# Kernel optimization log

Hardware: AMD Instinct MI355X
Metric: run time of the kernel (lower is better)

## Reference

```python
import jax, jax.numpy as jnp
import numpy as np

N = 100000      # nodes
E = 1600000     # edges
HID = 128
NODE_IN = 32
EDGE_IN = 16
EMB = 32
VOCAB = 100000
LAYERS = 3
EPS = 1e-5


def setup_inputs() -> dict:
    key = jax.random.key(0)
    ks = jax.random.split(key, 24)
    s = 0.05
    inp = {
        "x": jax.random.normal(ks[0], (N, NODE_IN), jnp.float32),
        "edge_attr": jax.random.normal(ks[1], (E, EDGE_IN), jnp.float32),
        "naics_emb": jax.random.normal(ks[2], (VOCAB, EMB), jnp.float32) * s,
        "ln_g": jnp.ones((EMB,), jnp.float32),
        "ln_b": jnp.zeros((EMB,), jnp.float32),
        "W_in": jax.random.normal(ks[3], (EMB + NODE_IN, HID), jnp.float32) * s,
        "b_in": jnp.zeros((HID,), jnp.float32),
        "Wl": jax.random.normal(ks[4], (LAYERS, HID, HID), jnp.float32) * s,
        "bl": jnp.zeros((LAYERS, HID), jnp.float32),
        "Wr": jax.random.normal(ks[5], (LAYERS, HID, HID), jnp.float32) * s,
        "bn_g": jnp.ones((LAYERS, HID), jnp.float32),
        "bn_b": jnp.zeros((LAYERS, HID), jnp.float32),
        "We1": jax.random.normal(ks[6], (2 * HID + EDGE_IN, HID), jnp.float32) * s,
        "be1": jnp.zeros((HID,), jnp.float32),
        "We2": jax.random.normal(ks[7], (HID, HID // 2), jnp.float32) * s,
        "be2": jnp.zeros((HID // 2,), jnp.float32),
        "We3": jax.random.normal(ks[8], (HID // 2, 1), jnp.float32) * s,
        "be3": jnp.zeros((1,), jnp.float32),
        "edge_index": jax.random.randint(ks[9], (2, E), 0, N, jnp.int64 if jax.config.jax_enable_x64 else jnp.int32),
        "naics_indices": jax.random.randint(ks[10], (N,), 0, VOCAB, jnp.int64 if jax.config.jax_enable_x64 else jnp.int32),
    }
    return inp


def reference(x, edge_attr, naics_emb, ln_g, ln_b, W_in, b_in, Wl, bl, Wr,
              bn_g, bn_b, We1, be1, We2, be2, We3, be3, edge_index, naics_indices):
    # NAICS embedding + LayerNorm
    emb = naics_emb[naics_indices]                    # [N, EMB]
    mu = emb.mean(-1, keepdims=True)
    var = emb.var(-1, keepdims=True)
    emb = (emb - mu) * jax.lax.rsqrt(var + EPS) * ln_g + ln_b

    # input projection (dropout in eval mode = identity)
    h = jax.nn.relu(jnp.concatenate([emb, x], axis=1) @ W_in + b_in)  # [N, HID]
    initial = h

    row, col = edge_index[0], edge_index[1]           # src, dst (PyG: aggregate at dst)
    deg = jax.ops.segment_sum(jnp.ones((E,), h.dtype), col, num_segments=N)
    inv_deg = (1.0 / jnp.maximum(deg, 1.0))[:, None]  # [N,1]

    for i in range(LAYERS):
        # SAGEConv: lin_l(mean_j x_j) + lin_r(x_i)
        agg = jax.ops.segment_sum(h[row], col, num_segments=N) * inv_deg
        out = agg @ Wl[i] + bl[i] + h @ Wr[i]
        # BatchNorm1d (training-mode batch statistics over nodes)
        m = out.mean(0)
        v = out.var(0)
        out = (out - m) * jax.lax.rsqrt(v + EPS) * bn_g[i] + bn_b[i]
        h = jnp.tanh(out) + h                         # activation + residual
        if i % 2 == 1:
            h = h + initial

    # edge-gather MLP
    ef = jnp.concatenate([h[row], h[col], edge_attr], axis=1)  # [E, 2H+EDGE_IN]
    z = jax.nn.relu(ef @ We1 + be1)
    z = jax.nn.relu(z @ We2 + be2)
    return z @ We3 + be3                              # [E, 1]
```

## Files before the change

### kernel.cpp

```cpp
#include <hip/hip_runtime.h>
#include <hip/hip_bf16.h>
#include <cstddef>

#define HID 128
#define EMBD 32
#define NIN 32
#define EIN 16
#define EPSV 1e-5f

__device__ __forceinline__ float rlf(float v, int l) {
    return __int_as_float(__builtin_amdgcn_readlane(__float_as_int(v), l));
}

extern "C" __global__ void __launch_bounds__(256)
k_input(const float* __restrict__ x, const float* __restrict__ etab,
        const int* __restrict__ nidx, const float* __restrict__ lng_,
        const float* __restrict__ lnb_, const float* __restrict__ Win,
        const float* __restrict__ bin_, float* __restrict__ h,
        float* __restrict__ init_, int nn)
{
    __shared__ float Ws[64 * HID];
    __shared__ float lng[EMBD], lnb[EMBD], bin[HID];
    __shared__ float xbuf[4][64];
    for (int i = threadIdx.x; i < 64 * HID; i += 256) Ws[i] = Win[i];
    if (threadIdx.x < EMBD) { lng[threadIdx.x] = lng_[threadIdx.x]; lnb[threadIdx.x] = lnb_[threadIdx.x]; }
    if (threadIdx.x < HID) bin[threadIdx.x] = bin_[threadIdx.x];
    __syncthreads();
    const int wv = threadIdx.x >> 6, lane = threadIdx.x & 63;
    const int w0 = blockIdx.x * 4 + wv, nw = gridDim.x * 4;
    for (int n = w0; n < nn; n += nw) {
        float e = 0.f;
        if (lane < EMBD) e = etab[(size_t)nidx[n] * EMBD + lane];
        float s = e, q = e * e;
        #pragma unroll
        for (int o = 16; o; o >>= 1) { s += __shfl_xor(s, o, 32); q += __shfl_xor(q, o, 32); }
        if (lane < EMBD) {
            float m = s * (1.f / EMBD);
            float v = q * (1.f / EMBD) - m * m;
            xbuf[wv][lane] = (e - m) * rsqrtf(v + EPSV) * lng[lane] + lnb[lane];
        } else {
            xbuf[wv][lane] = x[(size_t)n * NIN + (lane - NIN)];
        }
        float2 a0 = *(const float2*)&bin[2 * lane], a1 = {0.f, 0.f};
        #pragma unroll 8
        for (int k = 0; k < 64; k += 2) {
            float2 wA = *(const float2*)&Ws[k * HID + 2 * lane];
            float2 wB = *(const float2*)&Ws[(k + 1) * HID + 2 * lane];
            a0.x = fmaf(xbuf[wv][k], wA.x, a0.x);     a0.y = fmaf(xbuf[wv][k], wA.y, a0.y);
            a1.x = fmaf(xbuf[wv][k + 1], wB.x, a1.x); a1.y = fmaf(xbuf[wv][k + 1], wB.y, a1.y);
        }
        float2 r; r.x = fmaxf(a0.x + a1.x, 0.f); r.y = fmaxf(a0.y + a1.y, 0.f);
        *(float2*)&h[(size_t)n * HID + 2 * lane] = r;
        *(float2*)&init_[(size_t)n * HID + 2 * lane] = r;
    }
}

extern "C" __global__ void k_deg(const int* __restrict__ col, int* __restrict__ degi, int ne) {
    int i = blockIdx.x * blockDim.x + threadIdx.x, st = gridDim.x * blockDim.x;
    for (; i < ne; i += st) atomicAdd(&degi[col[i]], 1);
}

extern "C" __global__ void __launch_bounds__(1024)
k_scan(const int* __restrict__ degi, int* __restrict__ offs, int nn) {
    __shared__ int ps[1024];
    const int t = threadIdx.x;
    const int per = (nn + 1023) / 1024;
    const int s = min(t * per, nn), e = min(s + per, nn);
    int sum = 0;
    for (int i = s; i < e; i++) sum += degi[i];
    ps[t] = sum;
    __syncthreads();
    for (int off = 1; off < 1024; off <<= 1) {
        int v = (t >= off) ? ps[t - off] : 0;
        __syncthreads();
        ps[t] += v;
        __syncthreads();
    }
    int run = (t ? ps[t - 1] : 0);
    for (int i = s; i < e; i++) { offs[i] = run; run += degi[i]; }
    if (t == 1023) offs[nn] = run;
}

extern "C" __global__ void k_fill(const int* __restrict__ row, const int* __restrict__ col,
                                  const int* __restrict__ offs, int* __restrict__ cur,
                                  int* __restrict__ csr, int ne) {
    int i = blockIdx.x * blockDim.x + threadIdx.x, st = gridDim.x * blockDim.x;
    for (; i < ne; i += st) {
        int c = col[i];
        int p = atomicAdd(&cur[c], 1);
        csr[offs[c] + p] = row[i];
    }
}

extern "C" __global__ void __launch_bounds__(256)
k_agg(const float* __restrict__ h, const int* __restrict__ offs,
      const int* __restrict__ csr, float* __restrict__ agg, int nn)
{
    const int lane = threadIdx.x & 63;
    int w = blockIdx.x * 4 + (threadIdx.x >> 6), nw = gridDim.x * 4;
    for (int n = w; n < nn; n += nw) {
        const int nu = __builtin_amdgcn_readfirstlane(n);
        const int o0 = offs[nu], o1 = offs[nu + 1];
        float2 acc = {0.f, 0.f};
        int j = o0;
        for (; j + 4 <= o1; j += 4) {
            int s0 = csr[j], s1 = csr[j + 1], s2 = csr[j + 2], s3 = csr[j + 3];
            float2 v0 = *(const float2*)&h[(size_t)s0 * HID + 2 * lane];
            float2 v1 = *(const float2*)&h[(size_t)s1 * HID + 2 * lane];
            float2 v2 = *(const float2*)&h[(size_t)s2 * HID + 2 * lane];
            float2 v3 = *(const float2*)&h[(size_t)s3 * HID + 2 * lane];
            acc.x += (v0.x + v1.x) + (v2.x + v3.x);
            acc.y += (v0.y + v1.y) + (v2.y + v3.y);
        }
        for (; j < o1; j++) {
            int s0 = csr[j];
            float2 v0 = *(const float2*)&h[(size_t)s0 * HID + 2 * lane];
            acc.x += v0.x; acc.y += v0.y;
        }
        const float idg = 1.f / fmaxf((float)(o1 - o0), 1.f);
        float2 r; r.x = acc.x * idg; r.y = acc.y * idg;
        *(float2*)&agg[(size_t)n * HID + 2 * lane] = r;
    }
}

extern "C" __global__ void k_degf(const int* __restrict__ col, float* __restrict__ deg, int ne) {
    int i = blockIdx.x * blockDim.x + threadIdx.x, st = gridDim.x * blockDim.x;
    for (; i < ne; i += st) unsafeAtomicAdd(&deg[col[i]], 1.f);
}
extern "C" __global__ void k_invdeg(const float* __restrict__ deg, float* __restrict__ inv, int nn) {
    int i = blockIdx.x * blockDim.x + threadIdx.x;
    if (i < nn) inv[i] = 1.f / fmaxf(deg[i], 1.f);
}
extern "C" __global__ void __launch_bounds__(256)
k_scatter(const float* __restrict__ h, const int* __restrict__ row,
          const int* __restrict__ col, float* agg, int ne)
{
    const int lane = threadIdx.x & 63;
    int w = blockIdx.x * 4 + (threadIdx.x >> 6), nw = gridDim.x * 4;
    for (int e = w; e < ne; e += nw) {
        int r = row[e], c = col[e];
        float2 v = *(const float2*)&h[(size_t)r * HID + 2 * lane];
        unsafeAtomicAdd(&agg[(size_t)c * HID + 2 * lane], v.x);
        unsafeAtomicAdd(&agg[(size_t)c * HID + 2 * lane + 1], v.y);
    }
}

extern "C" __global__ void __launch_bounds__(512)
k_gemm(const float* __restrict__ X1, const float* __restrict__ scale,
       const float* __restrict__ W1, const float* __restrict__ X2,
       const float* __restrict__ W2, const float* __restrict__ bias,
       float* __restrict__ out, float* __restrict__ stats, int nn)
{
    __shared__ float W1s[HID * HID];
    __shared__ float W2s[HID * HID];
    const int tid = threadIdx.x;
    const bool dual = (X2 != nullptr);
    for (int i = tid; i < HID * HID / 4; i += 512) {
        ((float4*)W1s)[i] = ((const float4*)W1)[i];
        if (dual) ((float4*)W2s)[i] = ((const float4*)W2)[i];
    }
    __syncthreads();
    const int lane = tid & 63, wv = tid >> 6;
    const int gw = blockIdx.x * 8 + wv, nwv = gridDim.x * 8;
    float2 bv = {0.f, 0.f};
    if (bias) bv = *(const float2*)&bias[2 * lane];
    float2 sm = {0.f, 0.f}, sq = {0.f, 0.f};
    for (int nb = gw * 8; nb < nn; nb += nwv * 8) {
        const int nN = min(8, nn - nb);
        float2 xA[8], xB[8];
        #pragma unroll
        for (int i = 0; i < 8; i++) {
            xA[i] = {0.f, 0.f}; xB[i] = {0.f, 0.f};
            if (i < nN) {
                xA[i] = *(const float2*)&X1[(size_t)(nb + i) * HID + 2 * lane];
                if (scale) { float sc = scale[nb + i]; xA[i].x *= sc; xA[i].y *= sc; }
                if (dual) xB[i] = *(const float2*)&X2[(size_t)(nb + i) * HID + 2 * lane];
            }
        }
        float2 acc[8];
        #pragma unroll
        for (int i = 0; i < 8; i++) acc[i] = bv;
        if (dual) {
            for (int k = 0; k < HID; k += 2) {
                float2 w1a = *(const float2*)&W1s[k * HID + 2 * lane];
                float2 w1b = *(const float2*)&W1s[(k + 1) * HID + 2 * lane];
                float2 w2a = *(const float2*)&W2s[k * HID + 2 * lane];
                float2 w2b = *(const float2*)&W2s[(k + 1) * HID + 2 * lane];
                const int kl = k >> 1;
                #pragma unroll
                for (int i = 0; i < 8; i++) {
                    float sa = rlf(xA[i].x, kl), sb = rlf(xA[i].y, kl);
                    float ta = rlf(xB[i].x, kl), tb = rlf(xB[i].y, kl);
                    acc[i].x = fmaf(sa, w1a.x, acc[i].x); acc[i].y = fmaf(sa, w1a.y, acc[i].y);
                    acc[i].x = fmaf(sb, w1b.x, acc[i].x); acc[i].y = fmaf(sb, w1b.y, acc[i].y);
                    acc[i].x = fmaf(ta, w2a.x, acc[i].x); acc[i].y = fmaf(ta, w2a.y, acc[i].y);
                    acc[i].x = fmaf(tb, w2b.x, acc[i].x); acc[i].y = fmaf(tb, w2b.y, acc[i].y);
                }
            }
        } else {
            for (int k = 0; k < HID; k += 2) {
                float2 w1a = *(const float2*)&W1s[k * HID + 2 * lane];
                float2 w1b = *(const float2*)&W1s[(k + 1) * HID + 2 * lane];
                const int kl = k >> 1;
                #pragma unroll
                for (int i = 0; i < 8; i++) {
                    float sa = rlf(xA[i].x, kl), sb = rlf(xA[i].y, kl);
                    acc[i].x = fmaf(sa, w1a.x, acc[i].x); acc[i].y = fmaf(sa, w1a.y, acc[i].y);
                    acc[i].x = fmaf(sb, w1b.x, acc[i].x); acc[i].y = fmaf(sb, w1b.y, acc[i].y);
                }
            }
        }
        #pragma unroll
        for (int i = 0; i < 8; i++) {
            if (i < nN) {
                *(float2*)&out[(size_t)(nb + i) * HID + 2 * lane] = acc[i];
                if (stats) {
                    sm.x += acc[i].x; sm.y += acc[i].y;
                    sq.x += acc[i].x * acc[i].x; sq.y += acc[i].y * acc[i].y;
                }
            }
        }
    }
    if (stats) {
        unsafeAtomicAdd(&stats[2 * lane],           sm.x);
        unsafeAtomicAdd(&stats[2 * lane + 1],       sm.y);
        unsafeAtomicAdd(&stats[HID + 2 * lane],     sq.x);
        unsafeAtomicAdd(&stats[HID + 2 * lane + 1], sq.y);
    }
}

extern "C" __global__ void k_bnfin(const float* __restrict__ stats, const float* __restrict__ g,
                                   const float* __restrict__ b, float* __restrict__ scsh, float invn)
{
    int f = threadIdx.x;
    if (f < HID) {
        float m = stats[f] * invn;
        float v = stats[HID + f] * invn - m * m;
        float s = rsqrtf(v + EPSV) * g[f];
        scsh[f] = s;
        scsh[HID + f] = fmaf(-m, s, b[f]);
    }
}

extern "C" __global__ void __launch_bounds__(256)
k_update(const float* __restrict__ outb, const float* __restrict__ scsh,
         float* h, const float* __restrict__ init_, int addinit, int n4)
{
    int i = blockIdx.x * blockDim.x + threadIdx.x, st = gridDim.x * blockDim.x;
    for (; i < n4; i += st) {
        float4 o = ((const float4*)outb)[i];
        int f = (i & 31) * 4;
        float4 s  = *(const float4*)&scsh[f];
        float4 sh = *(const float4*)&scsh[HID + f];
        float4 hv = ((const float4*)h)[i];
        float4 r;
        r.x = tanhf(fmaf(o.x, s.x, sh.x)) + hv.x;
        r.y = tanhf(fmaf(o.y, s.y, sh.y)) + hv.y;
        r.z = tanhf(fmaf(o.z, s.z, sh.z)) + hv.z;
        r.w = tanhf(fmaf(o.w, s.w, sh.w)) + hv.w;
        if (addinit) {
            float4 iv = ((const float4*)init_)[i];
            r.x += iv.x; r.y += iv.y; r.z += iv.z; r.w += iv.w;
        }
        ((float4*)h)[i] = r;
    }
}

extern "C" __global__ void __launch_bounds__(256)
k_edge(const float* __restrict__ A, const float* __restrict__ B,
       const float* __restrict__ eattr, const int* __restrict__ row,
       const int* __restrict__ col, const float* __restrict__ We1e,
       const float* __restrict__ We2, const float* __restrict__ be2,
       const float* __restrict__ We3, const float* __restrict__ be3,
       float* __restrict__ outp, int ne)
{
    __shared__ float zbuf[32][132];
    __shared__ float tbuf[4][32][8];
    const int tid = threadIdx.x, lane = tid & 63, wv = tid >> 6;
    float2 w1r[16];
    #pragma unroll
    for (int j = 0; j < 16; j++) w1r[j] = *(const float2*)&We1e[j * HID + 2 * lane];
    const int fi = lane & 7, ks = lane >> 3;
    const int f0 = 16 * wv + 2 * fi;
    float w2r0[16], w2r1[16];
    #pragma unroll
    for (int m = 0; m < 16; m++) {
        w2r0[m] = We2[(16 * ks + m) * 64 + f0];
        w2r1[m] = We2[(16 * ks + m) * 64 + f0 + 1];
    }
    const float b20 = be2[f0], b21 = be2[f0 + 1];
    const float w30 = We3[f0], w31 = We3[f0 + 1];
    const float bias3 = be3[0];
    const int wcol4 = (((lane >> 1) & 3) << 3) | ((lane >> 1) >> 2);
    const int woff = wcol4 * 4 + (lane & 1) * 2;
    for (int cb = blockIdx.x * 32; cb < ne; cb += gridDim.x * 32) {
        const int e0 = cb + wv * 8;
        float2 ear = {0.f, 0.f};
        if (e0 + (lane >> 3) < ne) ear = *(const float2*)&eattr[(size_t)e0 * EIN + 2 * lane];
        int rr[8], cc[8];
        #pragma unroll
        for (int i = 0; i < 8; i++) {
            const int e = e0 + i;
            rr[i] = (e < ne) ? row[e] : 0;
            cc[i] = (e < ne) ? col[e] : 0;
        }
        float2 av[8], bv8[8];
        #pragma unroll
        for (int i = 0; i < 8; i++) {
            av[i]  = *(const float2*)&A[(size_t)rr[i] * HID + 2 * lane];
            bv8[i] = *(const float2*)&B[(size_t)cc[i] * HID + 2 * lane];
        }
        #pragma unroll
        for (int i = 0; i < 8; i++) {
            float2 q; q.x = av[i].x + bv8[i].x; q.y = av[i].y + bv8[i].y;
            #pragma unroll
            for (int j = 0; j < 16; j++) {
                float s = rlf((j & 1) ? ear.y : ear.x, i * 8 + (j >> 1));
                q.x = fmaf(s, w1r[j].x, q.x);
                q.y = fmaf(s, w1r[j].y, q.y);
            }
            q.x = fmaxf(q.x, 0.f); q.y = fmaxf(q.y, 0.f);
            *(float2*)&zbuf[wv * 8 + i][woff] = q;
        }
        __syncthreads();
        #pragma unroll 2
        for (int e = 0; e < 32; e++) {
            float acc0 = 0.f, acc1 = 0.f;
            #pragma unroll
            for (int t = 0; t < 4; t++) {
                float4 z = *(const float4*)&zbuf[e][(t * 8 + ks) * 4];
                acc0 = fmaf(z.x, w2r0[4 * t + 0], acc0);
                acc0 = fmaf(z.y, w2r0[4 * t + 1], acc0);
                acc0 = fmaf(z.z, w2r0[4 * t + 2], acc0);
                acc0 = fmaf(z.w, w2r0[4 * t + 3], acc0);
                acc1 = fmaf(z.x, w2r1[4 * t + 0], acc1);
                acc1 = fmaf(z.y, w2r1[4 * t + 1], acc1);
                acc1 = fmaf(z.z, w2r1[4 * t + 2], acc1);
                acc1 = fmaf(z.w, w2r1[4 * t + 3], acc1);
            }
            acc0 += __shfl_xor(acc0, 8);  acc1 += __shfl_xor(acc1, 8);
            acc0 += __shfl_xor(acc0, 16); acc1 += __shfl_xor(acc1, 16);
            acc0 += __shfl_xor(acc0, 32); acc1 += __shfl_xor(acc1, 32);
            float o0 = fmaxf(acc0 + b20, 0.f), o1 = fmaxf(acc1 + b21, 0.f);
            float t3 = fmaf(o0, w30, o1 * w31);
            if (ks == 0) tbuf[wv][e][fi] = t3;
        }
        __syncthreads();
        {
            const int e = tid >> 3, p = tid & 7;
            float s = (tbuf[0][e][p] + tbuf[1][e][p]) + (tbuf[2][e][p] + tbuf[3][e][p]);
            s += __shfl_xor(s, 1); s += __shfl_xor(s, 2); s += __shfl_xor(s, 4);
            if (p == 0 && cb + e < ne) outp[cb + e] = s + bias3;
        }
        __syncthreads();
    }
}

extern "C" void kernel_launch(void* const* d_in, const int* in_sizes, int n_in,
                              void* d_out, int out_size, void* d_ws, size_t ws_size,
                              hipStream_t stream)
{
    const float* x     = (const float*)d_in[0];
    const float* eattr = (const float*)d_in[1];
    const float* etab  = (const float*)d_in[2];
    const float* lng   = (const float*)d_in[3];
    const float* lnb   = (const float*)d_in[4];
    const float* Win   = (const float*)d_in[5];
    const float* bin   = (const float*)d_in[6];
    const float* Wl    = (const float*)d_in[7];
    const float* bl    = (const float*)d_in[8];
    const float* Wr    = (const float*)d_in[9];
    const float* bng   = (const float*)d_in[10];
    const float* bnb   = (const float*)d_in[11];
    const float* We1   = (const float*)d_in[12];
    const float* be1   = (const float*)d_in[13];
    const float* We2   = (const float*)d_in[14];
    const float* be2   = (const float*)d_in[15];
    const float* We3   = (const float*)d_in[16];
    const float* be3   = (const float*)d_in[17];
    const int*   eidx  = (const int*)d_in[18];
    const int*   nidx  = (const int*)d_in[19];

    const int nn = in_sizes[0] / NIN;
    const int ne = in_sizes[1] / EIN;
    const int* row = eidx;
    const int* col = eidx + ne;

    float* ws = (float*)d_ws;
    const size_t big = (size_t)nn * HID;
    float* h    = ws;
    float* bufB = ws + big;
    float* bufA = ws + 2 * big;
    float* tail = ws + 3 * big;

    const size_t need_csr = (3 * big + 3 * (size_t)nn + 1 + (size_t)ne + 512) * 4;
    const bool use_csr = (ws_size >= need_csr);

    k_input<<<512, 256, 0, stream>>>(x, etab, nidx, lng, lnb, Win, bin, h, bufB, nn);

    if (use_csr) {
        int*   degi  = (int*)tail;
        int*   offs  = degi + nn;
        int*   cur   = offs + nn + 1;
        int*   csr   = cur + nn;
        float* stats = (float*)(csr + ne);
        float* scsh  = stats + 2 * HID;

        hipMemsetAsync(degi, 0, (size_t)nn * 4, stream);
        hipMemsetAsync(cur, 0, (size_t)nn * 4, stream);
        k_deg<<<1024, 256, 0, stream>>>(col, degi, ne);
        k_scan<<<1, 1024, 0, stream>>>(degi, offs, nn);
        k_fill<<<1024, 256, 0, stream>>>(row, col, offs, cur, csr, ne);

        for (int i = 0; i < 3; i++) {
            hipMemsetAsync(stats, 0, 2 * HID * 4, stream);
            k_agg<<<2048, 256, 0, stream>>>(h, offs, csr, bufA, nn);
            k_gemm<<<256, 512, 0, stream>>>(bufA, nullptr, Wl + (size_t)i * HID * HID,
                                            h, Wr + (size_t)i * HID * HID, bl + i * HID,
                                            bufA, stats, nn);
            k_bnfin<<<1, 128, 0, stream>>>(stats, bng + i * HID, bnb + i * HID, scsh, 1.0f / nn);
            k_update<<<1024, 256, 0, stream>>>(bufA, scsh, h, bufB, i & 1, nn * HID / 4);
        }

        k_gemm<<<256, 512, 0, stream>>>(h, nullptr, We1, nullptr, nullptr, be1, bufA, nullptr, nn);
        k_gemm<<<256, 512, 0, stream>>>(h, nullptr, We1 + HID * HID, nullptr, nullptr, nullptr, bufB, nullptr, nn);
    } else {
        float* deg   = tail;
        float* inv   = deg + nn;
        float* stats = inv + nn;
        float* scsh  = stats + 2 * HID;

        hipMemsetAsync(deg, 0, (size_t)nn * 4, stream);
        k_degf<<<1024, 256, 0, stream>>>(col, deg, ne);
        k_invdeg<<<(nn + 255) / 256, 256, 0, stream>>>(deg, inv, nn);

        for (int i = 0; i < 3; i++) {
            hipMemsetAsync(bufA, 0, big * 4, stream);
            hipMemsetAsync(stats, 0, 2 * HID * 4, stream);
            k_scatter<<<2048, 256, 0, stream>>>(h, row, col, bufA, ne);
            k_gemm<<<256, 512, 0, stream>>>(bufA, inv, Wl + (size_t)i * HID * HID,
                                            h, Wr + (size_t)i * HID * HID, bl + i * HID,
                                            bufA, stats, nn);
            k_bnfin<<<1, 128, 0, stream>>>(stats, bng + i * HID, bnb + i * HID, scsh, 1.0f / nn);
            k_update<<<1024, 256, 0, stream>>>(bufA, scsh, h, bufB, i & 1, nn * HID / 4);
        }

        k_gemm<<<256, 512, 0, stream>>>(h, nullptr, We1, nullptr, nullptr, be1, bufA, nullptr, nn);
        k_gemm<<<256, 512, 0, stream>>>(h, nullptr, We1 + HID * HID, nullptr, nullptr, nullptr, bufB, nullptr, nn);
    }

    k_edge<<<2560, 256, 0, stream>>>(bufA, bufB, eattr, row, col,
                                     We1 + 2 * HID * HID, We2, be2, We3, be3,
                                     (float*)d_out, ne);
}
```

Baseline: 3.003 ms.

## Software-pipeline edge MLP gathers, widen CSR aggregation unroll, enlarge GEMM blocks

The edge kernel now prefetches the next chunk's row/col indices, edge attributes and the gathered node projections while the current chunk runs its second and third MLP stages, overlapping gather latency with compute. The CSR mean aggregation unrolls 8 neighbours with two accumulators, drops readfirstlane, and launches more blocks to raise memory-level parallelism. The node GEMM uses 1024-thread blocks instead of 512, with 16 waves sharing the staged weights. The prefetch adds register pressure that may cut occupancy, and the larger GEMM blocks change how work is scheduled across CUs.

```diff
diff --git a/kernel.cpp b/kernel.cpp
--- a/kernel.cpp
+++ b/kernel.cpp
@@ -99,26 +99,29 @@
     const int lane = threadIdx.x & 63;
     int w = blockIdx.x * 4 + (threadIdx.x >> 6), nw = gridDim.x * 4;
     for (int n = w; n < nn; n += nw) {
-        const int nu = __builtin_amdgcn_readfirstlane(n);
-        const int o0 = offs[nu], o1 = offs[nu + 1];
-        float2 acc = {0.f, 0.f};
+        const int o0 = offs[n], o1 = offs[n + 1];
+        float2 acc0 = {0.f, 0.f}, acc1 = {0.f, 0.f};
         int j = o0;
-        for (; j + 4 <= o1; j += 4) {
-            int s0 = csr[j], s1 = csr[j + 1], s2 = csr[j + 2], s3 = csr[j + 3];
-            float2 v0 = *(const float2*)&h[(size_t)s0 * HID + 2 * lane];
-            float2 v1 = *(const float2*)&h[(size_t)s1 * HID + 2 * lane];
-            float2 v2 = *(const float2*)&h[(size_t)s2 * HID + 2 * lane];
-            float2 v3 = *(const float2*)&h[(size_t)s3 * HID + 2 * lane];
-            acc.x += (v0.x + v1.x) + (v2.x + v3.x);
-            acc.y += (v0.y + v1.y) + (v2.y + v3.y);
+        for (; j + 8 <= o1; j += 8) {
+            int s[8];
+            #pragma unroll
+            for (int i = 0; i < 8; i++) s[i] = csr[j + i];
+            float2 v[8];
+            #pragma unroll
+            for (int i = 0; i < 8; i++) v[i] = *(const float2*)&h[(size_t)s[i] * HID + 2 * lane];
+            #pragma unroll
+            for (int i = 0; i < 8; i += 2) {
+                acc0.x += v[i].x;     acc0.y += v[i].y;
+                acc1.x += v[i + 1].x; acc1.y += v[i + 1].y;
+            }
         }
         for (; j < o1; j++) {
             int s0 = csr[j];
             float2 v0 = *(const float2*)&h[(size_t)s0 * HID + 2 * lane];
-            acc.x += v0.x; acc.y += v0.y;
+            acc0.x += v0.x; acc0.y += v0.y;
         }
         const float idg = 1.f / fmaxf((float)(o1 - o0), 1.f);
-        float2 r; r.x = acc.x * idg; r.y = acc.y * idg;
+        float2 r; r.x = (acc0.x + acc1.x) * idg; r.y = (acc0.y + acc1.y) * idg;
         *(float2*)&agg[(size_t)n * HID + 2 * lane] = r;
     }
 }
@@ -145,7 +148,7 @@
     }
 }
 
-extern "C" __global__ void __launch_bounds__(512)
+extern "C" __global__ void __launch_bounds__(1024)
 k_gemm(const float* __restrict__ X1, const float* __restrict__ scale,
        const float* __restrict__ W1, const float* __restrict__ X2,
        const float* __restrict__ W2, const float* __restrict__ bias,
@@ -155,13 +158,13 @@
     __shared__ float W2s[HID * HID];
     const int tid = threadIdx.x;
     const bool dual = (X2 != nullptr);
-    for (int i = tid; i < HID * HID / 4; i += 512) {
+    for (int i = tid; i < HID * HID / 4; i += 1024) {
         ((float4*)W1s)[i] = ((const float4*)W1)[i];
         if (dual) ((float4*)W2s)[i] = ((const float4*)W2)[i];
     }
     __syncthreads();
     const int lane = tid & 63, wv = tid >> 6;
-    const int gw = blockIdx.x * 8 + wv, nwv = gridDim.x * 8;
+    const int gw = blockIdx.x * 16 + wv, nwv = gridDim.x * 16;
     float2 bv = {0.f, 0.f};
     if (bias) bv = *(const float2*)&bias[2 * lane];
     float2 sm = {0.f, 0.f}, sq = {0.f, 0.f};
@@ -293,23 +296,29 @@
     const float bias3 = be3[0];
     const int wcol4 = (((lane >> 1) & 3) << 3) | ((lane >> 1) >> 2);
     const int woff = wcol4 * 4 + (lane & 1) * 2;
-    for (int cb = blockIdx.x * 32; cb < ne; cb += gridDim.x * 32) {
-        const int e0 = cb + wv * 8;
-        float2 ear = {0.f, 0.f};
-        if (e0 + (lane >> 3) < ne) ear = *(const float2*)&eattr[(size_t)e0 * EIN + 2 * lane];
-        int rr[8], cc[8];
-        #pragma unroll
-        for (int i = 0; i < 8; i++) {
-            const int e = e0 + i;
-            rr[i] = (e < ne) ? row[e] : 0;
-            cc[i] = (e < ne) ? col[e] : 0;
-        }
-        float2 av[8], bv8[8];
-        #pragma unroll
-        for (int i = 0; i < 8; i++) {
-            av[i]  = *(const float2*)&A[(size_t)rr[i] * HID + 2 * lane];
-            bv8[i] = *(const float2*)&B[(size_t)cc[i] * HID + 2 * lane];
-        }
+    const int stride = gridDim.x * 32;
+
+    float2 ear, av[8], bv8[8];
+
+#define PREF(cbase)                                                            \
+    {                                                                          \
+        const int e0p = (cbase) + wv * 8;                                      \
+        ear = make_float2(0.f, 0.f);                                           \
+        if (e0p + (lane >> 3) < ne)                                            \
+            ear = *(const float2*)&eattr[(size_t)e0p * EIN + 2 * lane];        \
+        _Pragma("unroll")                                                      \
+        for (int i = 0; i < 8; i++) {                                          \
+            const int e = e0p + i;                                             \
+            const int r = (e < ne) ? row[e] : 0;                               \
+            const int c = (e < ne) ? col[e] : 0;                               \
+            av[i]  = *(const float2*)&A[(size_t)r * HID + 2 * lane];           \
+            bv8[i] = *(const float2*)&B[(size_t)c * HID + 2 * lane];           \
+        }                                                                      \
+    }
+
+    int cb = blockIdx.x * 32;
+    if (cb < ne) PREF(cb);
+    for (; cb < ne; cb += stride) {
         #pragma unroll
         for (int i = 0; i < 8; i++) {
             float2 q; q.x = av[i].x + bv8[i].x; q.y = av[i].y + bv8[i].y;
@@ -323,7 +332,7 @@
             *(float2*)&zbuf[wv * 8 + i][woff] = q;
         }
         __syncthreads();
-        #pragma unroll 2
+        if (cb + stride < ne) PREF(cb + stride);
         for (int e = 0; e < 32; e++) {
             float acc0 = 0.f, acc1 = 0.f;
             #pragma unroll
@@ -354,6 +363,7 @@
         }
         __syncthreads();
     }
+#undef PREF
 }
 
 extern "C" void kernel_launch(void* const* d_in, const int* in_sizes, int n_in,
@@ -414,16 +424,16 @@
 
         for (int i = 0; i < 3; i++) {
             hipMemsetAsync(stats, 0, 2 * HID * 4, stream);
-            k_agg<<<2048, 256, 0, stream>>>(h, offs, csr, bufA, nn);
-            k_gemm<<<256, 512, 0, stream>>>(bufA, nullptr, Wl + (size_t)i * HID * HID,
-                                            h, Wr + (size_t)i * HID * HID, bl + i * HID,
-                                            bufA, stats, nn);
+            k_agg<<<6400, 256, 0, stream>>>(h, offs, csr, bufA, nn);
+            k_gemm<<<256, 1024, 0, stream>>>(bufA, nullptr, Wl + (size_t)i * HID * HID,
+                                             h, Wr + (size_t)i * HID * HID, bl + i * HID,
+                                             bufA, stats, nn);
             k_bnfin<<<1, 128, 0, stream>>>(stats, bng + i * HID, bnb + i * HID, scsh, 1.0f / nn);
             k_update<<<1024, 256, 0, stream>>>(bufA, scsh, h, bufB, i & 1, nn * HID / 4);
         }
 
-        k_gemm<<<256, 512, 0, stream>>>(h, nullptr, We1, nullptr, nullptr, be1, bufA, nullptr, nn);
-        k_gemm<<<256, 512, 0, stream>>>(h, nullptr, We1 + HID * HID, nullptr, nullptr, nullptr, bufB, nullptr, nn);
+        k_gemm<<<256, 1024, 0, stream>>>(h, nullptr, We1, nullptr, nullptr, be1, bufA, nullptr, nn);
+        k_gemm<<<256, 1024, 0, stream>>>(h, nullptr, We1 + HID * HID, nullptr, nullptr, nullptr, bufB, nullptr, nn);
     } else {
         float* deg   = tail;
         float* inv   = deg + nn;
@@ -438,15 +448,15 @@
             hipMemsetAsync(bufA, 0, big * 4, stream);
             hipMemsetAsync(stats, 0, 2 * HID * 4, stream);
             k_scatter<<<2048, 256, 0, stream>>>(h, row, col, bufA, ne);
-            k_gemm<<<256, 512, 0, stream>>>(bufA, inv, Wl + (size_t)i * HID * HID,
-                                            h, Wr + (size_t)i * HID * HID, bl + i * HID,
-                                            bufA, stats, nn);
+            k_gemm<<<256, 1024, 0, stream>>>(bufA, inv, Wl + (size_t)i * HID * HID,
+                                             h, Wr + (size_t)i * HID * HID, bl + i * HID,
+                                             bufA, stats, nn);
             k_bnfin<<<1, 128, 0, stream>>>(stats, bng + i * HID, bnb + i * HID, scsh, 1.0f / nn);
             k_update<<<1024, 256, 0, stream>>>(bufA, scsh, h, bufB, i & 1, nn * HID / 4);
         }
 
-        k_gemm<<<256, 512, 0, stream>>>(h, nullptr, We1, nullptr, nullptr, be1, bufA, nullptr, nn);
-        k_gemm<<<256, 512, 0, stream>>>(h, nullptr, We1 + HID * HID, nullptr, nullptr, nullptr, bufB, nullptr, nn);
+        k_gemm<<<256, 1024, 0, stream>>>(h, nullptr, We1, nullptr, nullptr, be1, bufA, nullptr, nn);
+        k_gemm<<<256, 1024, 0, stream>>>(h, nullptr, We1 + HID * HID, nullptr, nullptr, nullptr, bufB, nullptr, nn);
     }
 
     k_edge<<<2560, 256, 0, stream>>>(bufA, bufB, eattr, row, col,
```

Measured after the change: 3.282 ms. +9.3%, slower.

## Fuse BN finalize, memsets and final projections into neighboring kernels

Applied to the files above, without the earlier changes.

Zeroing of the degree counters moves into the input kernel, and zeroing of the BN stats moves into the aggregation and scatter kernels, which removes the memset calls. BN finalization is folded into the update kernel. The last layer's BN, tanh and residual are fused with both We1 node projections in a new k_proj kernel, so the final h is never written back and the two separate GEMM launches go away. The aggregation loop is unrolled to 8 neighbours with two accumulators, and the edge kernel's second-layer inner loop uses pointer-stepped float4 loads. The edge kernel is also split into two launches over halves of the edge range with a smaller grid, which adds a launch and may change occupancy behaviour.

```diff
diff --git a/kernel.cpp b/kernel.cpp
--- a/kernel.cpp
+++ b/kernel.cpp
@@ -17,11 +17,15 @@
         const int* __restrict__ nidx, const float* __restrict__ lng_,
         const float* __restrict__ lnb_, const float* __restrict__ Win,
         const float* __restrict__ bin_, float* __restrict__ h,
-        float* __restrict__ init_, int nn)
+        float* __restrict__ init_, int* __restrict__ zi, int* __restrict__ zc, int nn)
 {
     __shared__ float Ws[64 * HID];
     __shared__ float lng[EMBD], lnb[EMBD], bin[HID];
     __shared__ float xbuf[4][64];
+    if (zi) {
+        int gid = blockIdx.x * blockDim.x + threadIdx.x, st = gridDim.x * blockDim.x;
+        for (int i = gid; i < nn; i += st) { zi[i] = 0; zc[i] = 0; }
+    }
     for (int i = threadIdx.x; i < 64 * HID; i += 256) Ws[i] = Win[i];
     if (threadIdx.x < EMBD) { lng[threadIdx.x] = lng_[threadIdx.x]; lnb[threadIdx.x] = lnb_[threadIdx.x]; }
     if (threadIdx.x < HID) bin[threadIdx.x] = bin_[threadIdx.x];
@@ -94,31 +98,36 @@
 
 extern "C" __global__ void __launch_bounds__(256)
 k_agg(const float* __restrict__ h, const int* __restrict__ offs,
-      const int* __restrict__ csr, float* __restrict__ agg, int nn)
-{
+      const int* __restrict__ csr, float* __restrict__ agg,
+      float* __restrict__ stats, int nn)
+{
+    if (blockIdx.x == 0 && threadIdx.x < 2 * HID) stats[threadIdx.x] = 0.f;
     const int lane = threadIdx.x & 63;
     int w = blockIdx.x * 4 + (threadIdx.x >> 6), nw = gridDim.x * 4;
     for (int n = w; n < nn; n += nw) {
-        const int nu = __builtin_amdgcn_readfirstlane(n);
-        const int o0 = offs[nu], o1 = offs[nu + 1];
-        float2 acc = {0.f, 0.f};
+        const int o0 = offs[n], o1 = offs[n + 1];
+        float2 acc0 = {0.f, 0.f}, acc1 = {0.f, 0.f};
         int j = o0;
-        for (; j + 4 <= o1; j += 4) {
-            int s0 = csr[j], s1 = csr[j + 1], s2 = csr[j + 2], s3 = csr[j + 3];
-            float2 v0 = *(const float2*)&h[(size_t)s0 * HID + 2 * lane];
-            float2 v1 = *(const float2*)&h[(size_t)s1 * HID + 2 * lane];
-            float2 v2 = *(const float2*)&h[(size_t)s2 * HID + 2 * lane];
-            float2 v3 = *(const float2*)&h[(size_t)s3 * HID + 2 * lane];
-            acc.x += (v0.x + v1.x) + (v2.x + v3.x);
-            acc.y += (v0.y + v1.y) + (v2.y + v3.y);
+        for (; j + 8 <= o1; j += 8) {
+            int s[8];
+            #pragma unroll
+            for (int i = 0; i < 8; i++) s[i] = csr[j + i];
+            float2 v[8];
+            #pragma unroll
+            for (int i = 0; i < 8; i++) v[i] = *(const float2*)&h[(size_t)s[i] * HID + 2 * lane];
+            #pragma unroll
+            for (int i = 0; i < 8; i += 2) {
+                acc0.x += v[i].x;     acc0.y += v[i].y;
+                acc1.x += v[i + 1].x; acc1.y += v[i + 1].y;
+            }
         }
         for (; j < o1; j++) {
             int s0 = csr[j];
             float2 v0 = *(const float2*)&h[(size_t)s0 * HID + 2 * lane];
-            acc.x += v0.x; acc.y += v0.y;
+            acc0.x += v0.x; acc0.y += v0.y;
         }
         const float idg = 1.f / fmaxf((float)(o1 - o0), 1.f);
-        float2 r; r.x = acc.x * idg; r.y = acc.y * idg;
+        float2 r; r.x = (acc0.x + acc1.x) * idg; r.y = (acc0.y + acc1.y) * idg;
         *(float2*)&agg[(size_t)n * HID + 2 * lane] = r;
     }
 }
@@ -133,8 +142,9 @@
 }
 extern "C" __global__ void __launch_bounds__(256)
 k_scatter(const float* __restrict__ h, const int* __restrict__ row,
-          const int* __restrict__ col, float* agg, int ne)
-{
+          const int* __restrict__ col, float* agg, float* __restrict__ stats, int ne)
+{
+    if (blockIdx.x == 0 && threadIdx.x < 2 * HID) stats[threadIdx.x] = 0.f;
     const int lane = threadIdx.x & 63;
     int w = blockIdx.x * 4 + (threadIdx.x >> 6), nw = gridDim.x * 4;
     for (int e = w; e < ne; e += nw) {
@@ -214,38 +224,32 @@
         for (int i = 0; i < 8; i++) {
             if (i < nN) {
                 *(float2*)&out[(size_t)(nb + i) * HID + 2 * lane] = acc[i];
-                if (stats) {
-                    sm.x += acc[i].x; sm.y += acc[i].y;
-                    sq.x += acc[i].x * acc[i].x; sq.y += acc[i].y * acc[i].y;
-                }
-            }
-        }
-    }
-    if (stats) {
-        unsafeAtomicAdd(&stats[2 * lane],           sm.x);
-        unsafeAtomicAdd(&stats[2 * lane + 1],       sm.y);
-        unsafeAtomicAdd(&stats[HID + 2 * lane],     sq.x);
-        unsafeAtomicAdd(&stats[HID + 2 * lane + 1], sq.y);
-    }
-}
-
-extern "C" __global__ void k_bnfin(const float* __restrict__ stats, const float* __restrict__ g,
-                                   const float* __restrict__ b, float* __restrict__ scsh, float invn)
-{
-    int f = threadIdx.x;
-    if (f < HID) {
+                sm.x += acc[i].x; sm.y += acc[i].y;
+                sq.x += acc[i].x * acc[i].x; sq.y += acc[i].y * acc[i].y;
+            }
+        }
+    }
+    unsafeAtomicAdd(&stats[2 * lane],           sm.x);
+    unsafeAtomicAdd(&stats[2 * lane + 1],       sm.y);
+    unsafeAtomicAdd(&stats[HID + 2 * lane],     sq.x);
+    unsafeAtomicAdd(&stats[HID + 2 * lane + 1], sq.y);
+}
+
+extern "C" __global__ void __launch_bounds__(256)
+k_update(const float* __restrict__ outb, const float* __restrict__ stats,
+         const float* __restrict__ g, const float* __restrict__ b,
+         float* h, const float* __restrict__ init_, int addinit, int n4, float invn)
+{
+    __shared__ float scsh[2 * HID];
+    if (threadIdx.x < HID) {
+        int f = threadIdx.x;
         float m = stats[f] * invn;
         float v = stats[HID + f] * invn - m * m;
         float s = rsqrtf(v + EPSV) * g[f];
         scsh[f] = s;
         scsh[HID + f] = fmaf(-m, s, b[f]);
     }
-}
-
-extern "C" __global__ void __launch_bounds__(256)
-k_update(const float* __restrict__ outb, const float* __restrict__ scsh,
-         float* h, const float* __restrict__ init_, int addinit, int n4)
-{
+    __syncthreads();
     int i = blockIdx.x * blockDim.x + threadIdx.x, st = gridDim.x * blockDim.x;
     for (; i < n4; i += st) {
         float4 o = ((const float4*)outb)[i];
@@ -266,13 +270,82 @@
     }
 }
 
+extern "C" __global__ void __launch_bounds__(512)
+k_proj(const float* __restrict__ outb, const float* __restrict__ stats,
+       const float* __restrict__ g, const float* __restrict__ b,
+       const float* __restrict__ hold, const float* __restrict__ W1,
+       const float* __restrict__ W2, const float* __restrict__ b1,
+       float* __restrict__ outA, float* __restrict__ outB, int nn, float invn)
+{
+    __shared__ float W1s[HID * HID];
+    __shared__ float W2s[HID * HID];
+    __shared__ float scsh[2 * HID];
+    const int tid = threadIdx.x;
+    for (int i = tid; i < HID * HID / 4; i += 512) {
+        ((float4*)W1s)[i] = ((const float4*)W1)[i];
+        ((float4*)W2s)[i] = ((const float4*)W2)[i];
+    }
+    if (tid < HID) {
+        float m = stats[tid] * invn;
+        float v = stats[HID + tid] * invn - m * m;
+        float s = rsqrtf(v + EPSV) * g[tid];
+        scsh[tid] = s;
+        scsh[HID + tid] = fmaf(-m, s, b[tid]);
+    }
+    __syncthreads();
+    const int lane = tid & 63, wv = tid >> 6;
+    const int gw = blockIdx.x * 8 + wv, nwv = gridDim.x * 8;
+    const float2 sA  = *(const float2*)&scsh[2 * lane];
+    const float2 shA = *(const float2*)&scsh[HID + 2 * lane];
+    float2 bv = *(const float2*)&b1[2 * lane];
+    for (int nb = gw * 8; nb < nn; nb += nwv * 8) {
+        const int nN = min(8, nn - nb);
+        float2 xH[8];
+        #pragma unroll
+        for (int i = 0; i < 8; i++) {
+            xH[i] = {0.f, 0.f};
+            if (i < nN) {
+                float2 o  = *(const float2*)&outb[(size_t)(nb + i) * HID + 2 * lane];
+                float2 hv = *(const float2*)&hold[(size_t)(nb + i) * HID + 2 * lane];
+                xH[i].x = tanhf(fmaf(o.x, sA.x, shA.x)) + hv.x;
+                xH[i].y = tanhf(fmaf(o.y, sA.y, shA.y)) + hv.y;
+            }
+        }
+        float2 accA[8], accB[8];
+        #pragma unroll
+        for (int i = 0; i < 8; i++) { accA[i] = bv; accB[i] = {0.f, 0.f}; }
+        for (int k = 0; k < HID; k += 2) {
+            float2 w1a = *(const float2*)&W1s[k * HID + 2 * lane];
+            float2 w1b = *(const float2*)&W1s[(k + 1) * HID + 2 * lane];
+            float2 w2a = *(const float2*)&W2s[k * HID + 2 * lane];
+            float2 w2b = *(const float2*)&W2s[(k + 1) * HID + 2 * lane];
+            const int kl = k >> 1;
+            #pragma unroll
+            for (int i = 0; i < 8; i++) {
+                float sa = rlf(xH[i].x, kl), sb = rlf(xH[i].y, kl);
+                accA[i].x = fmaf(sa, w1a.x, accA[i].x); accA[i].y = fmaf(sa, w1a.y, accA[i].y);
+                accA[i].x = fmaf(sb, w1b.x, accA[i].x); accA[i].y = fmaf(sb, w1b.y, accA[i].y);
+                accB[i].x = fmaf(sa, w2a.x, accB[i].x); accB[i].y = fmaf(sa, w2a.y, accB[i].y);
+                accB[i].x = fmaf(sb, w2b.x, accB[i].x); accB[i].y = fmaf(sb, w2b.y, accB[i].y);
+            }
+        }
+        #pragma unroll
+        for (int i = 0; i < 8; i++) {
+            if (i < nN) {
+                *(float2*)&outA[(size_t)(nb + i) * HID + 2 * lane] = accA[i];
+                *(float2*)&outB[(size_t)(nb + i) * HID + 2 * lane] = accB[i];
+            }
+        }
+    }
+}
+
 extern "C" __global__ void __launch_bounds__(256)
 k_edge(const float* __restrict__ A, const float* __restrict__ B,
        const float* __restrict__ eattr, const int* __restrict__ row,
        const int* __restrict__ col, const float* __restrict__ We1e,
        const float* __restrict__ We2, const float* __restrict__ be2,
        const float* __restrict__ We3, const float* __restrict__ be3,
-       float* __restrict__ outp, int ne)
+       float* __restrict__ outp, int beg, int end, int ne)
 {
     __shared__ float zbuf[32][132];
     __shared__ float tbuf[4][32][8];
@@ -293,7 +366,7 @@
     const float bias3 = be3[0];
     const int wcol4 = (((lane >> 1) & 3) << 3) | ((lane >> 1) >> 2);
     const int woff = wcol4 * 4 + (lane & 1) * 2;
-    for (int cb = blockIdx.x * 32; cb < ne; cb += gridDim.x * 32) {
+    for (int cb = beg + blockIdx.x * 32; cb < end; cb += gridDim.x * 32) {
         const int e0 = cb + wv * 8;
         float2 ear = {0.f, 0.f};
         if (e0 + (lane >> 3) < ne) ear = *(const float2*)&eattr[(size_t)e0 * EIN + 2 * lane];
@@ -310,6 +383,7 @@
             av[i]  = *(const float2*)&A[(size_t)rr[i] * HID + 2 * lane];
             bv8[i] = *(const float2*)&B[(size_t)cc[i] * HID + 2 * lane];
         }
+        float* zw = &zbuf[wv * 8][woff];
         #pragma unroll
         for (int i = 0; i < 8; i++) {
             float2 q; q.x = av[i].x + bv8[i].x; q.y = av[i].y + bv8[i].y;
@@ -320,24 +394,35 @@
                 q.y = fmaf(s, w1r[j].y, q.y);
             }
             q.x = fmaxf(q.x, 0.f); q.y = fmaxf(q.y, 0.f);
-            *(float2*)&zbuf[wv * 8 + i][woff] = q;
+            *(float2*)zw = q;
+            zw += 132;
         }
         __syncthreads();
+        const float* zp = &zbuf[0][ks * 4];
         #pragma unroll 2
         for (int e = 0; e < 32; e++) {
+            float4 z0 = *(const float4*)(zp);
+            float4 z1 = *(const float4*)(zp + 32);
+            float4 z2 = *(const float4*)(zp + 64);
+            float4 z3 = *(const float4*)(zp + 96);
+            zp += 132;
             float acc0 = 0.f, acc1 = 0.f;
-            #pragma unroll
-            for (int t = 0; t < 4; t++) {
-                float4 z = *(const float4*)&zbuf[e][(t * 8 + ks) * 4];
-                acc0 = fmaf(z.x, w2r0[4 * t + 0], acc0);
-                acc0 = fmaf(z.y, w2r0[4 * t + 1], acc0);
-                acc0 = fmaf(z.z, w2r0[4 * t + 2], acc0);
-                acc0 = fmaf(z.w, w2r0[4 * t + 3], acc0);
-                acc1 = fmaf(z.x, w2r1[4 * t + 0], acc1);
-                acc1 = fmaf(z.y, w2r1[4 * t + 1], acc1);
-                acc1 = fmaf(z.z, w2r1[4 * t + 2], acc1);
-                acc1 = fmaf(z.w, w2r1[4 * t + 3], acc1);
-            }
+            acc0 = fmaf(z0.x, w2r0[0],  acc0); acc1 = fmaf(z0.x, w2r1[0],  acc1);
+            acc0 = fmaf(z0.y, w2r0[1],  acc0); acc1 = fmaf(z0.y, w2r1[1],  acc1);
+            acc0 = fmaf(z0.z, w2r0[2],  acc0); acc1 = fmaf(z0.z, w2r1[2],  acc1);
+            acc0 = fmaf(z0.w, w2r0[3],  acc0); acc1 = fmaf(z0.w, w2r1[3],  acc1);
+            acc0 = fmaf(z1.x, w2r0[4],  acc0); acc1 = fmaf(z1.x, w2r1[4],  acc1);
+            acc0 = fmaf(z1.y, w2r0[5],  acc0); acc1 = fmaf(z1.y, w2r1[5],  acc1);
+            acc0 = fmaf(z1.z, w2r0[6],  acc0); acc1 = fmaf(z1.z, w2r1[6],  acc1);
+            acc0 = fmaf(z1.w, w2r0[7],  acc0); acc1 = fmaf(z1.w, w2r1[7],  acc1);
+            acc0 = fmaf(z2.x, w2r0[8],  acc0); acc1 = fmaf(z2.x, w2r1[8],  acc1);
+            acc0 = fmaf(z2.y, w2r0[9],  acc0); acc1 = fmaf(z2.y, w2r1[9],  acc1);
+            acc0 = fmaf(z2.z, w2r0[10], acc0); acc1 = fmaf(z2.z, w2r1[10], acc1);
+            acc0 = fmaf(z2.w, w2r0[11], acc0); acc1 = fmaf(z2.w, w2r1[11], acc1);
+            acc0 = fmaf(z3.x, w2r0[12], acc0); acc1 = fmaf(z3.x, w2r1[12], acc1);
+            acc0 = fmaf(z3.y, w2r0[13], acc0); acc1 = fmaf(z3.y, w2r1[13], acc1);
+            acc0 = fmaf(z3.z, w2r0[14], acc0); acc1 = fmaf(z3.z, w2r1[14], acc1);
+            acc0 = fmaf(z3.w, w2r0[15], acc0); acc1 = fmaf(z3.w, w2r1[15], acc1);
             acc0 += __shfl_xor(acc0, 8);  acc1 += __shfl_xor(acc1, 8);
             acc0 += __shfl_xor(acc0, 16); acc1 += __shfl_xor(acc1, 16);
             acc0 += __shfl_xor(acc0, 32); acc1 += __shfl_xor(acc1, 32);
@@ -350,7 +435,7 @@
             const int e = tid >> 3, p = tid & 7;
             float s = (tbuf[0][e][p] + tbuf[1][e][p]) + (tbuf[2][e][p] + tbuf[3][e][p]);
             s += __shfl_xor(s, 1); s += __shfl_xor(s, 2); s += __shfl_xor(s, 4);
-            if (p == 0 && cb + e < ne) outp[cb + e] = s + bias3;
+            if (p == 0 && cb + e < end) outp[cb + e] = s + bias3;
         }
         __syncthreads();
     }
@@ -385,6 +470,7 @@
     const int ne = in_sizes[1] / EIN;
     const int* row = eidx;
     const int* col = eidx + ne;
+    const float invn = 1.0f / nn;
 
     float* ws = (float*)d_ws;
     const size_t big = (size_t)nn * HID;
@@ -396,60 +482,66 @@
     const size_t need_csr = (3 * big + 3 * (size_t)nn + 1 + (size_t)ne + 512) * 4;
     const bool use_csr = (ws_size >= need_csr);
 
-    k_input<<<512, 256, 0, stream>>>(x, etab, nidx, lng, lnb, Win, bin, h, bufB, nn);
-
     if (use_csr) {
         int*   degi  = (int*)tail;
         int*   offs  = degi + nn;
         int*   cur   = offs + nn + 1;
         int*   csr   = cur + nn;
         float* stats = (float*)(csr + ne);
-        float* scsh  = stats + 2 * HID;
-
-        hipMemsetAsync(degi, 0, (size_t)nn * 4, stream);
-        hipMemsetAsync(cur, 0, (size_t)nn * 4, stream);
+
+        k_input<<<512, 256, 0, stream>>>(x, etab, nidx, lng, lnb, Win, bin, h, bufB,
+                                         degi, cur, nn);
         k_deg<<<1024, 256, 0, stream>>>(col, degi, ne);
         k_scan<<<1, 1024, 0, stream>>>(degi, offs, nn);
         k_fill<<<1024, 256, 0, stream>>>(row, col, offs, cur, csr, ne);
 
         for (int i = 0; i < 3; i++) {
-            hipMemsetAsync(stats, 0, 2 * HID * 4, stream);
-            k_agg<<<2048, 256, 0, stream>>>(h, offs, csr, bufA, nn);
+            k_agg<<<2048, 256, 0, stream>>>(h, offs, csr, bufA, stats, nn);
             k_gemm<<<256, 512, 0, stream>>>(bufA, nullptr, Wl + (size_t)i * HID * HID,
                                             h, Wr + (size_t)i * HID * HID, bl + i * HID,
                                             bufA, stats, nn);
-            k_bnfin<<<1, 128, 0, stream>>>(stats, bng + i * HID, bnb + i * HID, scsh, 1.0f / nn);
-            k_update<<<1024, 256, 0, stream>>>(bufA, scsh, h, bufB, i & 1, nn * HID / 4);
-        }
-
-        k_gemm<<<256, 512, 0, stream>>>(h, nullptr, We1, nullptr, nullptr, be1, bufA, nullptr, nn);
-        k_gemm<<<256, 512, 0, stream>>>(h, nullptr, We1 + HID * HID, nullptr, nullptr, nullptr, bufB, nullptr, nn);
+            if (i < 2) {
+                k_update<<<1024, 256, 0, stream>>>(bufA, stats, bng + i * HID, bnb + i * HID,
+                                                   h, bufB, i & 1, nn * HID / 4, invn);
+            } else {
+                k_proj<<<256, 512, 0, stream>>>(bufA, stats, bng + i * HID, bnb + i * HID,
+                                                h, We1, We1 + HID * HID, be1,
+                                                bufA, bufB, nn, invn);
+            }
+        }
     } else {
         float* deg   = tail;
         float* inv   = deg + nn;
         float* stats = inv + nn;
-        float* scsh  = stats + 2 * HID;
-
+
+        k_input<<<512, 256, 0, stream>>>(x, etab, nidx, lng, lnb, Win, bin, h, bufB,
+                                         nullptr, nullptr, nn);
         hipMemsetAsync(deg, 0, (size_t)nn * 4, stream);
         k_degf<<<1024, 256, 0, stream>>>(col, deg, ne);
         k_invdeg<<<(nn + 255) / 256, 256, 0, stream>>>(deg, inv, nn);
 
         for (int i = 0; i < 3; i++) {
             hipMemsetAsync(bufA, 0, big * 4, stream);
-            hipMemsetAsync(stats, 0, 2 * HID * 4, stream);
-            k_scatter<<<2048, 256, 0, stream>>>(h, row, col, bufA, ne);
+            k_scatter<<<2048, 256, 0, stream>>>(h, row, col, bufA, stats, ne);
             k_gemm<<<256, 512, 0, stream>>>(bufA, inv, Wl + (size_t)i * HID * HID,
                                             h, Wr + (size_t)i * HID * HID, bl + i * HID,
                                             bufA, stats, nn);
-            k_bnfin<<<1, 128, 0, stream>>>(stats, bng + i * HID, bnb + i * HID, scsh, 1.0f / nn);
-            k_update<<<1024, 256, 0, stream>>>(bufA, scsh, h, bufB, i & 1, nn * HID / 4);
-        }
-
-        k_gemm<<<256, 512, 0, stream>>>(h, nullptr, We1, nullptr, nullptr, be1, bufA, nullptr, nn);
-        k_gemm<<<256, 512, 0, stream>>>(h, nullptr, We1 + HID * HID, nullptr, nullptr, nullptr, bufB, nullptr, nn);
-    }
-
-    k_edge<<<2560, 256, 0, stream>>>(bufA, bufB, eattr, row, col,
+            if (i < 2) {
+                k_update<<<1024, 256, 0, stream>>>(bufA, stats, bng + i * HID, bnb + i * HID,
+                                                   h, bufB, i & 1, nn * HID / 4, invn);
+            } else {
+                k_proj<<<256, 512, 0, stream>>>(bufA, stats, bng + i * HID, bnb + i * HID,
+                                                h, We1, We1 + HID * HID, be1,
+                                                bufA, bufB, nn, invn);
+            }
+        }
+    }
+
+    const int half = (ne / 2) & ~31;
+    k_edge<<<1792, 256, 0, stream>>>(bufA, bufB, eattr, row, col,
                                      We1 + 2 * HID * HID, We2, be2, We3, be3,
-                                     (float*)d_out, ne);
-}
+                                     (float*)d_out, 0, half, ne);
+    k_edge<<<1792, 256, 0, stream>>>(bufA, bufB, eattr, row, col,
+                                     We1 + 2 * HID * HID, We2, be2, We3, be3,
+                                     (float*)d_out, half, ne, ne);
+}
```

After: 2.897 ms. -3.6%, faster.
